# Kernel optimization log

Hardware: AMD Instinct MI355X
Metric: run time of the kernel (lower is better)

Reference implementation:

```python
import jax, jax.numpy as jnp
import numpy as np

S, D = 8192, 2048      # sequence length, feature dim (input_size)
H, E, K, L = 64, 64, 2, 64  # gate hidden, expert count, top-k, expert layer_size
EPS = 1e-12            # torch F.normalize eps


def setup_inputs() -> dict:
    key = jax.random.key(0)
    ks = jax.random.split(key, 5)
    x = jax.random.normal(ks[0], (S, D), dtype=jnp.float32)
    # torch nn.Linear weights have shape [out_features, in_features]
    Wg_in = jax.random.normal(ks[1], (H, D), dtype=jnp.float32) * 0.02   # gate.input
    Wg_lin = jax.random.normal(ks[2], (E, H), dtype=jnp.float32) * 0.02  # gate.linear
    Wg_out = jax.random.normal(ks[3], (1, S), dtype=jnp.float32) * 0.02  # gate.output
    We = jax.random.normal(ks[4], (E, L, D), dtype=jnp.float32) * 0.02   # expert weight bank
    return {"x": x, "Wg_in": Wg_in, "Wg_lin": Wg_lin, "Wg_out": Wg_out, "We": We}


def reference(x, Wg_in, Wg_lin, Wg_out, We):
    # --- SparseGate (eval mode: dropout = identity) ---
    h = x @ Wg_in.T                         # [S, H]
    logits = h @ Wg_lin.T                   # [S, E]
    scores = (logits.T @ Wg_out.T)[:, 0]    # Linear(S,1) applied to [E,S] -> [E]
    topv, idx = jax.lax.top_k(scores, K)    # global top-k experts for whole input
    g = jax.nn.softmax(topv)                # softmax over the k selected logits

    # --- dispatch to k selected experts (FFNN: Linear -> normalize(-1) -> GELU) ---
    Wsel = We[idx]                          # [K, L, D]
    z = jnp.einsum('sd,kld->ksl', x, Wsel)  # [K, S, L]
    z = z / jnp.maximum(jnp.linalg.norm(z, axis=-1, keepdims=True), EPS)
    z = jax.nn.gelu(z, approximate=False)   # torch GELU default is exact erf

    # --- weighted combine: sum_k g_k * expert_k(x) ---
    return jnp.einsum('k,ksl->sl', g, z)    # [S, L]
```

## Files before the change

### kernel.cpp

```cpp
#include <hip/hip_runtime.h>
#include <hip/hip_bf16.h>
#include <math.h>

#define D_DIM 2048
#define L_DIM 64
#define E_NUM 64
#define H_DIM 64

typedef float f32x4_t __attribute__((ext_vector_type(4)));
typedef __bf16 bf16x8_t __attribute__((ext_vector_type(8)));

#define WS_UPART 0u
#define WS_U     (512u * 2048u * 4u)
#define WS_V     (WS_U + 2048u * 4u)
#define WS_META  (WS_V + 256u)
#define WS_WB    (WS_META + 64u)
#define WS_XB    (WS_WB + 128u * 2048u * 2u)
#define WS_PART  (WS_XB + 8192u * 2048u * 2u)

__global__ void k_upart(const float* __restrict__ x, const float* __restrict__ wout,
                        float* __restrict__ upart, __hip_bfloat16* __restrict__ xb) {
  const int d8 = threadIdx.x * 8;
  const int s0 = blockIdx.x * 16;
  float a0 = 0.f, a1 = 0.f, a2 = 0.f, a3 = 0.f;
  float a4 = 0.f, a5 = 0.f, a6 = 0.f, a7 = 0.f;
  for (int i = 0; i < 16; ++i) {
    const size_t row = (size_t)(s0 + i);
    const float w = wout[s0 + i];
    const float4 pa = *reinterpret_cast<const float4*>(x + row * D_DIM + d8);
    const float4 pb = *reinterpret_cast<const float4*>(x + row * D_DIM + d8 + 4);
    a0 += pa.x * w; a1 += pa.y * w; a2 += pa.z * w; a3 += pa.w * w;
    a4 += pb.x * w; a5 += pb.y * w; a6 += pb.z * w; a7 += pb.w * w;
    union { __hip_bfloat16 h[8]; uint4 u; } pk;
    pk.h[0] = __float2bfloat16(pa.x); pk.h[1] = __float2bfloat16(pa.y);
    pk.h[2] = __float2bfloat16(pa.z); pk.h[3] = __float2bfloat16(pa.w);
    pk.h[4] = __float2bfloat16(pb.x); pk.h[5] = __float2bfloat16(pb.y);
    pk.h[6] = __float2bfloat16(pb.z); pk.h[7] = __float2bfloat16(pb.w);
    *reinterpret_cast<uint4*>(xb + row * D_DIM + d8) = pk.u;
  }
  float* up = upart + (size_t)blockIdx.x * D_DIM + d8;
  *reinterpret_cast<float4*>(up)     = make_float4(a0, a1, a2, a3);
  *reinterpret_cast<float4*>(up + 4) = make_float4(a4, a5, a6, a7);
}

__global__ void k_ufinish(const float* __restrict__ upart, float* __restrict__ u) {
  const int d = blockIdx.x * 256 + threadIdx.x;
  float s = 0.f;
#pragma unroll 8
  for (int c = 0; c < 512; ++c) s += upart[(size_t)c * D_DIM + d];
  u[d] = s;
}

__global__ void k_v(const float* __restrict__ wg_in, const float* __restrict__ u,
                    float* __restrict__ v) {
  const int h = blockIdx.x;
  const int t = threadIdx.x;
  const float4* wr = reinterpret_cast<const float4*>(wg_in + (size_t)h * D_DIM);
  const float4* ur = reinterpret_cast<const float4*>(u);
  float s = 0.f;
#pragma unroll
  for (int i = t; i < 512; i += 256) {
    const float4 a = wr[i];
    const float4 b = ur[i];
    s += a.x * b.x + a.y * b.y + a.z * b.z + a.w * b.w;
  }
  __shared__ float red[4];
#pragma unroll
  for (int off = 32; off; off >>= 1) s += __shfl_down(s, off, 64);
  if ((t & 63) == 0) red[t >> 6] = s;
  __syncthreads();
  if (t == 0) v[h] = red[0] + red[1] + red[2] + red[3];
}

__global__ void k_gate(const float* __restrict__ wg_lin, const float* __restrict__ v,
                       int* __restrict__ sel, float* __restrict__ g) {
  __shared__ float vv[H_DIM];
  __shared__ float sc[E_NUM];
  const int t = threadIdx.x;
  vv[t] = v[t];
  __syncthreads();
  float s = 0.f;
#pragma unroll 8
  for (int hh = 0; hh < H_DIM; ++hh) s += wg_lin[t * H_DIM + hh] * vv[hh];
  sc[t] = s;
  __syncthreads();
  if (t == 0) {
    int b1 = 0; float m1 = sc[0];
    for (int e = 1; e < E_NUM; ++e) { if (sc[e] > m1) { m1 = sc[e]; b1 = e; } }
    int b2 = -1; float m2 = -3.4e38f;
    for (int e = 0; e < E_NUM; ++e) {
      if (e != b1 && sc[e] > m2) { m2 = sc[e]; b2 = e; }
    }
    const float e2 = expf(m2 - m1);
    const float g0 = 1.0f / (1.0f + e2);
    sel[0] = b1; sel[1] = b2;
    g[0] = g0; g[1] = 1.0f - g0;
  }
}

__global__ void k_wb(const float* __restrict__ we, const int* __restrict__ sel,
                     __hip_bfloat16* __restrict__ wb) {
  const int n = blockIdx.x;
  const int e = sel[n >> 6];
  const int l = n & 63;
  const float* src = we + ((size_t)e * L_DIM + l) * D_DIM;
  const int t = threadIdx.x;
  const float4 a = reinterpret_cast<const float4*>(src)[2 * t];
  const float4 b = reinterpret_cast<const float4*>(src)[2 * t + 1];
  union { __hip_bfloat16 h[8]; uint4 u; } pk;
  pk.h[0] = __float2bfloat16(a.x); pk.h[1] = __float2bfloat16(a.y);
  pk.h[2] = __float2bfloat16(a.z); pk.h[3] = __float2bfloat16(a.w);
  pk.h[4] = __float2bfloat16(b.x); pk.h[5] = __float2bfloat16(b.y);
  pk.h[6] = __float2bfloat16(b.z); pk.h[7] = __float2bfloat16(b.w);
  reinterpret_cast<uint4*>(wb + (size_t)n * D_DIM)[t] = pk.u;
}

__device__ __forceinline__ void async_ld16(const void* gp, void* lp) {
  __builtin_amdgcn_global_load_lds(
      (const __attribute__((address_space(1))) unsigned int*)gp,
      (__attribute__((address_space(3))) unsigned int*)lp, 16, 0, 0);
}

__device__ __forceinline__ float gelu_f(float v) {
  return 0.5f * v * (1.0f + erff(v * 0.70710678118654752440f));
}

__global__ __launch_bounds__(512) void k_moe_gemm(
    const __hip_bfloat16* __restrict__ xb, const __hip_bfloat16* __restrict__ wb,
    float* __restrict__ part) {
  __shared__ __align__(16) unsigned char lds[2][32768];

  const int tid = threadIdx.x;
  const int w = tid >> 6, lane = tid & 63;
  const int wm = w >> 2, wn = w & 3;
  const int m0 = blockIdx.x * 128;
  const int kg = blockIdx.y;
  const int kbase = kg * 512;
  const int fr = lane & 15, fq = lane >> 4;

  int sr[2], skc[2];
#pragma unroll
  for (int ph = 0; ph < 2; ++ph) {
    const int c = ph * 512 + tid;
    sr[ph] = c >> 3;
    skc[ph] = (c & 7) ^ (sr[ph] & 7);
  }

  f32x4_t acc[4][2];
#pragma unroll
  for (int mf = 0; mf < 4; ++mf)
#pragma unroll
    for (int nf = 0; nf < 2; ++nf) acc[mf][nf] = (f32x4_t){0.f, 0.f, 0.f, 0.f};

  auto stage = [&](int buf, int kk) {
    const int koff = kbase + kk * 64;
#pragma unroll
    for (int ph = 0; ph < 2; ++ph) {
      const int c = ph * 512 + tid;
      async_ld16(xb + (size_t)(m0 + sr[ph]) * D_DIM + koff + skc[ph] * 8,
                 &lds[buf][c * 16]);
      async_ld16(wb + (size_t)sr[ph] * D_DIM + koff + skc[ph] * 8,
                 &lds[buf][16384 + c * 16]);
    }
  };

  stage(0, 0);
  __syncthreads();
  for (int kk = 0; kk < 8; ++kk) {
    const int cur = kk & 1;
    if (kk < 7) stage(cur ^ 1, kk + 1);
    const unsigned char* ldsA = lds[cur];
    const unsigned char* ldsB = lds[cur] + 16384;
    union fragu { uint4 u; bf16x8_t v; };
    fragu af[4][2], bf_[2][2];
#pragma unroll
    for (int mf = 0; mf < 4; ++mf)
#pragma unroll
      for (int ks = 0; ks < 2; ++ks) {
        const int ar = wm * 64 + mf * 16 + fr;
        const int kq = ks * 4 + fq;
        af[mf][ks].u = *reinterpret_cast<const uint4*>(
            ldsA + ar * 128 + ((kq ^ (ar & 7)) * 16));
      }
#pragma unroll
    for (int nf = 0; nf < 2; ++nf)
#pragma unroll
      for (int ks = 0; ks < 2; ++ks) {
        const int br = wn * 32 + nf * 16 + fr;
        const int kq = ks * 4 + fq;
        bf_[nf][ks].u = *reinterpret_cast<const uint4*>(
            ldsB + br * 128 + ((kq ^ (br & 7)) * 16));
      }
#pragma unroll
    for (int mf = 0; mf < 4; ++mf)
#pragma unroll
      for (int nf = 0; nf < 2; ++nf) {
        acc[mf][nf] = __builtin_amdgcn_mfma_f32_16x16x32_bf16(
            af[mf][0].v, bf_[nf][0].v, acc[mf][nf], 0, 0, 0);
        acc[mf][nf] = __builtin_amdgcn_mfma_f32_16x16x32_bf16(
            af[mf][1].v, bf_[nf][1].v, acc[mf][nf], 0, 0, 0);
      }
    __syncthreads();
  }

  float* z = reinterpret_cast<float*>(lds);
#pragma unroll
  for (int mf = 0; mf < 4; ++mf)
#pragma unroll
    for (int nf = 0; nf < 2; ++nf)
#pragma unroll
      for (int reg = 0; reg < 4; ++reg)
        z[(wm * 64 + mf * 16 + fq * 4 + reg) * 128 + wn * 32 + nf * 16 + fr] =
            acc[mf][nf][reg];
  __syncthreads();
#pragma unroll
  for (int p = 0; p < 8; ++p) {
    const int idx = p * 512 + tid;
    const int r = idx >> 5, c4 = (idx & 31) * 4;
    *reinterpret_cast<f32x4_t*>(part + ((size_t)kg * 8192 + m0 + r) * 128 + c4) =
        *reinterpret_cast<const f32x4_t*>(z + r * 128 + c4);
  }
}

__global__ __launch_bounds__(256) void k_finish(const float* __restrict__ part,
                                                const float* __restrict__ gw,
                                                float* __restrict__ out) {
  __shared__ float z[32 * 132];
  __shared__ float ps[32 * 8];
  const int tid = threadIdx.x;
  const int m0 = blockIdx.x * 32;
  const float g0 = gw[0], g1 = gw[1];
  const size_t KSTRIDE = (size_t)8192 * 128;
#pragma unroll
  for (int p = 0; p < 4; ++p) {
    const int idx = p * 256 + tid;
    const int r = idx >> 5, c4 = (idx & 31) * 4;
    const float* pp = part + ((size_t)(m0 + r)) * 128 + c4;
    const f32x4_t s = *reinterpret_cast<const f32x4_t*>(pp)
                    + *reinterpret_cast<const f32x4_t*>(pp + KSTRIDE)
                    + *reinterpret_cast<const f32x4_t*>(pp + 2 * KSTRIDE)
                    + *reinterpret_cast<const f32x4_t*>(pp + 3 * KSTRIDE);
    z[r * 132 + c4 + 0] = s[0];
    z[r * 132 + c4 + 1] = s[1];
    z[r * 132 + c4 + 2] = s[2];
    z[r * 132 + c4 + 3] = s[3];
  }
  __syncthreads();
  {
    const int r = tid >> 3, seg = tid & 7;
    float s = 0.f;
#pragma unroll
    for (int i2 = 0; i2 < 16; ++i2) {
      const float t2 = z[r * 132 + seg * 16 + i2];
      s += t2 * t2;
    }
    ps[r * 8 + seg] = s;
  }
  __syncthreads();
  {
    const int r = tid >> 3, j = tid & 7;
    const float s0 = ps[r * 8 + 0] + ps[r * 8 + 1] + ps[r * 8 + 2] + ps[r * 8 + 3];
    const float s1 = ps[r * 8 + 4] + ps[r * 8 + 5] + ps[r * 8 + 6] + ps[r * 8 + 7];
    const float i0 = 1.0f / fmaxf(sqrtf(s0), 1e-12f);
    const float i1 = 1.0f / fmaxf(sqrtf(s1), 1e-12f);
    float o[8];
#pragma unroll
    for (int i2 = 0; i2 < 8; ++i2) {
      const int c = j * 8 + i2;
      const float za = z[r * 132 + c] * i0;
      const float zb2 = z[r * 132 + 64 + c] * i1;
      o[i2] = g0 * gelu_f(za) + g1 * gelu_f(zb2);
    }
    float4* op = reinterpret_cast<float4*>(out + (size_t)(m0 + r) * 64 + j * 8);
    op[0] = make_float4(o[0], o[1], o[2], o[3]);
    op[1] = make_float4(o[4], o[5], o[6], o[7]);
  }
}

extern "C" void kernel_launch(void* const* d_in, const int* in_sizes, int n_in,
                              void* d_out, int out_size, void* d_ws, size_t ws_size,
                              hipStream_t stream) {
  (void)in_sizes; (void)n_in; (void)out_size; (void)ws_size;
  const float* x      = (const float*)d_in[0];
  const float* wg_in  = (const float*)d_in[1];
  const float* wg_lin = (const float*)d_in[2];
  const float* wg_out = (const float*)d_in[3];
  const float* we     = (const float*)d_in[4];
  float* out = (float*)d_out;
  char* ws = (char*)d_ws;

  float* upart = (float*)(ws + WS_UPART);
  float* u     = (float*)(ws + WS_U);
  float* v     = (float*)(ws + WS_V);
  int*   sel   = (int*)(ws + WS_META);
  float* g     = (float*)(ws + WS_META + 8);
  __hip_bfloat16* wb = (__hip_bfloat16*)(ws + WS_WB);
  __hip_bfloat16* xb = (__hip_bfloat16*)(ws + WS_XB);
  float* part = (float*)(ws + WS_PART);

  k_upart  <<<512, 256, 0, stream>>>(x, wg_out, upart, xb);
  k_ufinish<<<8, 256, 0, stream>>>(upart, u);
  k_v      <<<64, 256, 0, stream>>>(wg_in, u, v);
  k_gate   <<<1, 64, 0, stream>>>(wg_lin, v, sel, g);
  k_wb     <<<128, 256, 0, stream>>>(we, sel, wb);
  k_moe_gemm<<<dim3(64, 4), 512, 0, stream>>>(xb, wb, part);
  k_finish <<<256, 256, 0, stream>>>(part, g, out);
}
```

Before: 183.1 us.

## Pre-tile and pre-swizzle bf16 operands so GEMM stages contiguous LDS tiles

The bf16 conversion kernels now write x and the selected expert weights in a tiled layout. Each tile is 128 rows by 64 k and already carries the XOR swizzle the LDS layout expects. The GEMM's async global-to-LDS loads then become fully contiguous 16-byte chunks, which removes the per-thread row/column address math and the strided row accesses. The trade-off is scattered 16-byte stores in the producer kernels, whose write coalescing may suffer.

```diff
diff --git a/kernel.cpp b/kernel.cpp
--- a/kernel.cpp
+++ b/kernel.cpp
@@ -18,17 +18,21 @@
 #define WS_XB    (WS_WB + 128u * 2048u * 2u)
 #define WS_PART  (WS_XB + 8192u * 2048u * 2u)
 
+
 __global__ void k_upart(const float* __restrict__ x, const float* __restrict__ wout,
-                        float* __restrict__ upart, __hip_bfloat16* __restrict__ xb) {
-  const int d8 = threadIdx.x * 8;
+                        float* __restrict__ upart, __hip_bfloat16* __restrict__ xbt) {
+  const int t = threadIdx.x;
+  const int d8 = t * 8;
   const int s0 = blockIdx.x * 16;
+  const int kstep = d8 >> 6;
+  const int kc = (d8 >> 3) & 7;
   float a0 = 0.f, a1 = 0.f, a2 = 0.f, a3 = 0.f;
   float a4 = 0.f, a5 = 0.f, a6 = 0.f, a7 = 0.f;
   for (int i = 0; i < 16; ++i) {
-    const size_t row = (size_t)(s0 + i);
-    const float w = wout[s0 + i];
-    const float4 pa = *reinterpret_cast<const float4*>(x + row * D_DIM + d8);
-    const float4 pb = *reinterpret_cast<const float4*>(x + row * D_DIM + d8 + 4);
+    const int row = s0 + i;
+    const float w = wout[row];
+    const float4 pa = *reinterpret_cast<const float4*>(x + (size_t)row * D_DIM + d8);
+    const float4 pb = *reinterpret_cast<const float4*>(x + (size_t)row * D_DIM + d8 + 4);
     a0 += pa.x * w; a1 += pa.y * w; a2 += pa.z * w; a3 += pa.w * w;
     a4 += pb.x * w; a5 += pb.y * w; a6 += pb.z * w; a7 += pb.w * w;
     union { __hip_bfloat16 h[8]; uint4 u; } pk;
@@ -36,7 +40,10 @@
     pk.h[2] = __float2bfloat16(pa.z); pk.h[3] = __float2bfloat16(pa.w);
     pk.h[4] = __float2bfloat16(pb.x); pk.h[5] = __float2bfloat16(pb.y);
     pk.h[6] = __float2bfloat16(pb.z); pk.h[7] = __float2bfloat16(pb.w);
-    *reinterpret_cast<uint4*>(xb + row * D_DIM + d8) = pk.u;
+    const int mt = row >> 7, rl = row & 127;
+    const size_t off = (size_t)mt * 262144 + kstep * 8192 + rl * 64 +
+                       ((kc ^ (rl & 7)) * 8);
+    *reinterpret_cast<uint4*>(xbt + off) = pk.u;
   }
   float* up = upart + (size_t)blockIdx.x * D_DIM + d8;
   *reinterpret_cast<float4*>(up)     = make_float4(a0, a1, a2, a3);
@@ -99,12 +106,15 @@
 }
 
 __global__ void k_wb(const float* __restrict__ we, const int* __restrict__ sel,
-                     __hip_bfloat16* __restrict__ wb) {
+                     __hip_bfloat16* __restrict__ wbt) {
   const int n = blockIdx.x;
   const int e = sel[n >> 6];
   const int l = n & 63;
   const float* src = we + ((size_t)e * L_DIM + l) * D_DIM;
   const int t = threadIdx.x;
+  const int d8 = t * 8;
+  const int kstep = d8 >> 6;
+  const int kc = (d8 >> 3) & 7;
   const float4 a = reinterpret_cast<const float4*>(src)[2 * t];
   const float4 b = reinterpret_cast<const float4*>(src)[2 * t + 1];
   union { __hip_bfloat16 h[8]; uint4 u; } pk;
@@ -112,7 +122,8 @@
   pk.h[2] = __float2bfloat16(a.z); pk.h[3] = __float2bfloat16(a.w);
   pk.h[4] = __float2bfloat16(b.x); pk.h[5] = __float2bfloat16(b.y);
   pk.h[6] = __float2bfloat16(b.z); pk.h[7] = __float2bfloat16(b.w);
-  reinterpret_cast<uint4*>(wb + (size_t)n * D_DIM)[t] = pk.u;
+  const size_t off = (size_t)kstep * 8192 + n * 64 + ((kc ^ (n & 7)) * 8);
+  *reinterpret_cast<uint4*>(wbt + off) = pk.u;
 }
 
 __device__ __forceinline__ void async_ld16(const void* gp, void* lp) {
@@ -126,7 +137,7 @@
 }
 
 __global__ __launch_bounds__(512) void k_moe_gemm(
-    const __hip_bfloat16* __restrict__ xb, const __hip_bfloat16* __restrict__ wb,
+    const __hip_bfloat16* __restrict__ xbt, const __hip_bfloat16* __restrict__ wbt,
     float* __restrict__ part) {
   __shared__ __align__(16) unsigned char lds[2][32768];
 
@@ -135,16 +146,8 @@
   const int wm = w >> 2, wn = w & 3;
   const int m0 = blockIdx.x * 128;
   const int kg = blockIdx.y;
-  const int kbase = kg * 512;
   const int fr = lane & 15, fq = lane >> 4;
-
-  int sr[2], skc[2];
-#pragma unroll
-  for (int ph = 0; ph < 2; ++ph) {
-    const int c = ph * 512 + tid;
-    sr[ph] = c >> 3;
-    skc[ph] = (c & 7) ^ (sr[ph] & 7);
-  }
+  const size_t abase = (size_t)blockIdx.x * 262144;
 
   f32x4_t acc[4][2];
 #pragma unroll
@@ -153,14 +156,12 @@
     for (int nf = 0; nf < 2; ++nf) acc[mf][nf] = (f32x4_t){0.f, 0.f, 0.f, 0.f};
 
   auto stage = [&](int buf, int kk) {
-    const int koff = kbase + kk * 64;
+    const size_t tbase = (size_t)(kg * 8 + kk) * 8192;
 #pragma unroll
     for (int ph = 0; ph < 2; ++ph) {
       const int c = ph * 512 + tid;
-      async_ld16(xb + (size_t)(m0 + sr[ph]) * D_DIM + koff + skc[ph] * 8,
-                 &lds[buf][c * 16]);
-      async_ld16(wb + (size_t)sr[ph] * D_DIM + koff + skc[ph] * 8,
-                 &lds[buf][16384 + c * 16]);
+      async_ld16(xbt + abase + tbase + c * 8, &lds[buf][c * 16]);
+      async_ld16(wbt + tbase + c * 8, &lds[buf][16384 + c * 16]);
     }
   };
 
@@ -294,15 +295,15 @@
   float* v     = (float*)(ws + WS_V);
   int*   sel   = (int*)(ws + WS_META);
   float* g     = (float*)(ws + WS_META + 8);
-  __hip_bfloat16* wb = (__hip_bfloat16*)(ws + WS_WB);
-  __hip_bfloat16* xb = (__hip_bfloat16*)(ws + WS_XB);
+  __hip_bfloat16* wbt = (__hip_bfloat16*)(ws + WS_WB);
+  __hip_bfloat16* xbt = (__hip_bfloat16*)(ws + WS_XB);
   float* part = (float*)(ws + WS_PART);
 
-  k_upart  <<<512, 256, 0, stream>>>(x, wg_out, upart, xb);
+  k_upart  <<<512, 256, 0, stream>>>(x, wg_out, upart, xbt);
   k_ufinish<<<8, 256, 0, stream>>>(upart, u);
   k_v      <<<64, 256, 0, stream>>>(wg_in, u, v);
   k_gate   <<<1, 64, 0, stream>>>(wg_lin, v, sel, g);
-  k_wb     <<<128, 256, 0, stream>>>(we, sel, wb);
-  k_moe_gemm<<<dim3(64, 4), 512, 0, stream>>>(xb, wb, part);
+  k_wb     <<<128, 256, 0, stream>>>(we, sel, wbt);
+  k_moe_gemm<<<dim3(64, 4), 512, 0, stream>>>(xbt, wbt, part);
   k_finish <<<256, 256, 0, stream>>>(part, g, out);
 }
```

Result: no change. 184.2 us (+0.6%).
